# Kernel tuning notes

Hardware: AMD Instinct MI355X
Metric: run time of the kernel (lower is better)

## Reference

```python
import jax, jax.numpy as jnp
import numpy as np

N_NODES = 100000
N_EDGES = 1000000
IN_DIM = 64
HID = 64
OUT = 64
NEG_SLOPE = 0.2  # PyG GATConv default


def setup_inputs() -> dict:
    key = jax.random.key(0)
    ks = jax.random.split(key, 10)
    x = jax.random.normal(ks[0], (N_NODES, IN_DIM), dtype=jnp.float32)
    edge_index = jax.random.randint(ks[1], (2, N_EDGES), 0, N_NODES, dtype=jnp.int64)
    s = 1.0 / np.sqrt(IN_DIM)
    sh = 1.0 / np.sqrt(HID)
    W_src = jax.random.uniform(ks[2], (IN_DIM, HID), jnp.float32, -s, s)
    W_dst = jax.random.uniform(ks[3], (IN_DIM, HID), jnp.float32, -s, s)
    att_src = jax.random.uniform(ks[4], (HID,), jnp.float32, -sh, sh)
    att_dst = jax.random.uniform(ks[5], (HID,), jnp.float32, -sh, sh)
    bias = jnp.zeros((HID,), jnp.float32)
    W_lin = jax.random.uniform(ks[6], (HID, OUT), jnp.float32, -sh, sh)
    b_lin = jax.random.uniform(ks[7], (OUT,), jnp.float32, -sh, sh)
    return {"x": x, "edge_index": edge_index, "W_src": W_src, "W_dst": W_dst,
            "att_src": att_src, "att_dst": att_dst, "bias": bias,
            "W_lin": W_lin, "b_lin": b_lin}


def reference(x, edge_index, W_src, W_dst, att_src, att_dst, bias, W_lin, b_lin):
    src, tgt = edge_index[0], edge_index[1]
    # Bias-free linear projections (PyG GATConv with tuple in_channels)
    h_src = x @ W_src                      # [N, HID]
    h_dst = x @ W_dst                      # [N, HID]
    a_src = h_src @ att_src                # [N]
    a_dst = h_dst @ att_dst                # [N]
    # Per-edge attention logits: LeakyReLU(a_src[j] + a_dst[i])
    e = a_src[src] + a_dst[tgt]            # [E]
    e = jnp.where(e > 0, e, NEG_SLOPE * e)
    # Segment-softmax over incoming edges of each target node
    seg_max = jax.ops.segment_max(e, tgt, num_segments=N_NODES)  # [N]
    expw = jnp.exp(e - seg_max[tgt])                             # [E]
    denom = jax.ops.segment_sum(expw, tgt, num_segments=N_NODES)  # [N]
    alpha = expw / (denom[tgt] + 1e-16)                          # [E]
    # Scatter-aggregate weighted source features
    msgs = alpha[:, None] * h_src[src]                           # [E, HID]
    out = jax.ops.segment_sum(msgs, tgt, num_segments=N_NODES)   # [N, HID]
    out = out + bias
    # Final linear + ReLU
    return jax.nn.relu(out @ W_lin + b_lin)
```

## Files before the change

kernel.cpp:

```cpp
#include <hip/hip_runtime.h>
#include <hip/hip_fp16.h>
#include <math.h>

#define HID 64
#define CBITS 6
#define CSZ 64
#define MAXB 2048
#define CAP 832
#define CAPH 576
#define PB 896
#define MSB 256
#define XSTR 17

__device__ __forceinline__ float4 f4fma(float a, const float4 b, float4 c) {
    c.x = fmaf(a, b.x, c.x); c.y = fmaf(a, b.y, c.y);
    c.z = fmaf(a, b.z, c.z); c.w = fmaf(a, b.w, c.w);
    return c;
}

__global__ void init_kernel(const float* __restrict__ W_dst,
                            const float* __restrict__ att_dst,
                            float* __restrict__ vdst,
                            int* __restrict__ gcursor, int nbc) {
    if (blockIdx.x == 0 && threadIdx.x < HID) {
        int k = threadIdx.x;
        float acc = 0.0f;
#pragma unroll 8
        for (int h = 0; h < HID; ++h) acc = fmaf(W_dst[k * HID + h], att_dst[h], acc);
        vdst[k] = acc;
    }
    int stride = gridDim.x * blockDim.x;
    for (int i = blockIdx.x * blockDim.x + threadIdx.x; i < nbc; i += stride)
        gcursor[i] = i * CAP;
}

__global__ void __launch_bounds__(256)
mid_kernel(const float* __restrict__ x,
           const float* __restrict__ W_src,
           const float* __restrict__ att_src,
           const float* __restrict__ vdst,
           __half* __restrict__ h_half,
           float* __restrict__ a_src,
           float* __restrict__ a_dst, int N,
           const int* __restrict__ src, const int* __restrict__ tgt,
           int* __restrict__ gcursor, int* __restrict__ rec, int E, int nbc) {
    __shared__ __align__(16) char smraw[25600];
    const int t = threadIdx.x;

    if (blockIdx.x < PB) {
        float4* Ws4  = (float4*)smraw;
        float4* att4 = Ws4 + HID * 16;
        float4* vd4  = att4 + 16;
        float4* xs4f = vd4 + 16;

        for (int i = t; i < HID * 16; i += 256) Ws4[i] = ((const float4*)W_src)[i];
        if (t < 16) {
            att4[t] = ((const float4*)att_src)[t];
            vd4[t]  = ((const float4*)vdst)[t];
        }

        const int g0 = t >> 4;
        const int s = t & 15;
        const float4* x4 = (const float4*)x;
        uint2* h2 = (uint2*)h_half;

        for (int base = blockIdx.x * 32; base < N; base += PB * 32) {
            __syncthreads();
#pragma unroll
            for (int u = 0; u < 2; ++u) {
                int f = t + u * 256;
                int node = base + (f >> 4);
                xs4f[(f >> 4) * XSTR + (f & 15)] =
                    (node < N) ? x4[(long long)node * 16 + (f & 15)]
                               : make_float4(0, 0, 0, 0);
            }
            __syncthreads();

            const float4* xr0 = xs4f + g0 * XSTR;
            const float4* xr1 = xs4f + (g0 + 16) * XSTR;

            float4 acc0 = make_float4(0, 0, 0, 0);
            float4 acc1 = make_float4(0, 0, 0, 0);
#pragma unroll 4
            for (int kk = 0; kk < 16; ++kk) {
                float4 xv0 = xr0[kk];
                float4 xv1 = xr1[kk];
                float4 w0 = Ws4[(4 * kk + 0) * 16 + s];
                float4 w1 = Ws4[(4 * kk + 1) * 16 + s];
                float4 w2 = Ws4[(4 * kk + 2) * 16 + s];
                float4 w3 = Ws4[(4 * kk + 3) * 16 + s];
                acc0 = f4fma(xv0.x, w0, acc0);
                acc1 = f4fma(xv1.x, w0, acc1);
                acc0 = f4fma(xv0.y, w1, acc0);
                acc1 = f4fma(xv1.y, w1, acc1);
                acc0 = f4fma(xv0.z, w2, acc0);
                acc1 = f4fma(xv1.z, w2, acc1);
                acc0 = f4fma(xv0.w, w3, acc0);
                acc1 = f4fma(xv1.w, w3, acc1);
            }

            float4 av = att4[s], qv = vd4[s];
            float p0 = acc0.x * av.x + acc0.y * av.y + acc0.z * av.z + acc0.w * av.w;
            float p1 = acc1.x * av.x + acc1.y * av.y + acc1.z * av.z + acc1.w * av.w;
            float4 xq0 = xr0[s];
            float4 xq1 = xr1[s];
            float q0 = xq0.x * qv.x + xq0.y * qv.y + xq0.z * qv.z + xq0.w * qv.w;
            float q1 = xq1.x * qv.x + xq1.y * qv.y + xq1.z * qv.z + xq1.w * qv.w;
#pragma unroll
            for (int off = 1; off < 16; off <<= 1) {
                p0 += __shfl_xor(p0, off, 64);
                p1 += __shfl_xor(p1, off, 64);
                q0 += __shfl_xor(q0, off, 64);
                q1 += __shfl_xor(q1, off, 64);
            }

            int n0 = base + g0, n1 = base + g0 + 16;
            if (n0 < N) {
                __half2 lo = __float22half2_rn(make_float2(acc0.x, acc0.y));
                __half2 hi = __float22half2_rn(make_float2(acc0.z, acc0.w));
                uint2 pk; pk.x = *(unsigned*)&lo; pk.y = *(unsigned*)&hi;
                h2[(long long)n0 * 16 + s] = pk;
                if (s == 0) { a_src[n0] = p0; a_dst[n0] = q0; }
            }
            if (n1 < N) {
                __half2 lo = __float22half2_rn(make_float2(acc1.x, acc1.y));
                __half2 hi = __float22half2_rn(make_float2(acc1.z, acc1.w));
                uint2 pk; pk.x = *(unsigned*)&lo; pk.y = *(unsigned*)&hi;
                h2[(long long)n1 * 16 + s] = pk;
                if (s == 0) { a_src[n1] = p1; a_dst[n1] = q1; }
            }
        }
    } else {
        int* lh = (int*)smraw;
        const int bid = blockIdx.x - PB;

        for (int i = t; i < nbc; i += 256) lh[i] = 0;
        __syncthreads();
        int chunk = (E + MSB - 1) / MSB;
        int e0 = bid * chunk;
        int e1 = min(E, e0 + chunk);
        for (int e = e0 + t; e < e1; e += 256)
            atomicAdd(&lh[tgt[e] >> CBITS], 1);
        __syncthreads();
        for (int i = t; i < nbc; i += 256)
            if (lh[i]) lh[i] = atomicAdd(&gcursor[i], lh[i]);
        __syncthreads();
        for (int e = e0 + t; e < e1; e += 256) {
            int s = src[e], tg = tgt[e];
            int bi = tg >> CBITS;
            int pos = atomicAdd(&lh[bi], 1);
            if (pos < (bi + 1) * CAP)
                rec[pos] = (s << CBITS) | (tg & (CSZ - 1));
        }
    }
}

__global__ void __launch_bounds__(256)
sort_gather_kernel(const int* __restrict__ gcursor, const int* __restrict__ rec,
                   const __half* __restrict__ h_half,
                   const float* __restrict__ a_src, const float* __restrict__ a_dst,
                   const float* __restrict__ bias,
                   const float* __restrict__ W_lin, const float* __restrict__ b_lin,
                   float* __restrict__ out, int N) {
    __shared__ float4 Wl4[HID * 16];
    __shared__ float4 bs4[16], bl4[16];
    __shared__ int ssort[CAPH];
    __shared__ int hist[32];
    __shared__ int loff[33];
    __shared__ int cur[32];
    __shared__ int sd[32];

    const int t = threadIdx.x;
    for (int i = t; i < HID * 16; i += 256) Wl4[i] = ((const float4*)W_lin)[i];
    if (t < 16) {
        bs4[t] = ((const float4*)bias)[t];
        bl4[t] = ((const float4*)b_lin)[t];
    }

    const int bk = blockIdx.x >> 1;
    const int half = blockIdx.x & 1;
    const int node0 = (bk << CBITS) + half * 32;
    const int nn = min(32, N - node0);
    const int beg = bk * CAP;
    int cnt = gcursor[bk] - beg;
    if (cnt > CAP) cnt = CAP;

    if (t < 32) hist[t] = 0;
    __syncthreads();
    for (int j = t; j < cnt; j += 256) {
        int tl = rec[beg + j] & (CSZ - 1);
        if ((tl >> 5) == half) atomicAdd(&hist[tl & 31], 1);
    }
    __syncthreads();
    if (t < 32) sd[t] = hist[t];
    __syncthreads();
    for (int off = 1; off < 32; off <<= 1) {
        int v = (t < 32 && t >= off) ? sd[t - off] : 0;
        __syncthreads();
        if (t < 32) sd[t] += v;
        __syncthreads();
    }
    if (t < 32) {
        int e = sd[t] - hist[t];
        loff[t] = e; cur[t] = e;
        if (t == 31) loff[32] = min(sd[31], CAPH);
    }
    __syncthreads();
    for (int j = t; j < cnt; j += 256) {
        int r = rec[beg + j];
        int tl = r & (CSZ - 1);
        if ((tl >> 5) == half) {
            int pos = atomicAdd(&cur[tl & 31], 1);
            if (pos < CAPH) ssort[pos] = r >> CBITS;
        }
    }
    __syncthreads();

    const int lane = t & 63;
    const int w = t >> 6;
    const int g = lane >> 4;
    const int s = lane & 15;
    const int gbase = g << 4;
    const uint2* h2 = (const uint2*)h_half;
    float4* out4 = (float4*)out;

#pragma unroll 1
    for (int r2 = 0; r2 < 2; ++r2) {
        int nloc = w * 8 + r2 * 4 + g;
        int n = node0 + nloc;
        bool act = (nloc < nn);
        float adn = act ? a_dst[n] : 0.0f;
        int jb = min(loff[nloc], CAPH);
        int je = min(loff[nloc + 1], CAPH);

        float4 acc = make_float4(0, 0, 0, 0);
        float dsum = 0.0f;
        int j = jb;
        for (; j + 4 <= je; j += 4) {
            int s0 = ssort[j], s1 = ssort[j + 1], s2 = ssort[j + 2], s3 = ssort[j + 3];
            uint2 r0 = h2[(long long)s0 * 16 + s];
            uint2 r1 = h2[(long long)s1 * 16 + s];
            uint2 r2v = h2[(long long)s2 * 16 + s];
            uint2 r3 = h2[(long long)s3 * 16 + s];
            float v0 = a_src[s0] + adn, v1 = a_src[s1] + adn;
            float v2 = a_src[s2] + adn, v3 = a_src[s3] + adn;
            v0 = (v0 > 0.0f) ? v0 : 0.2f * v0;
            v1 = (v1 > 0.0f) ? v1 : 0.2f * v1;
            v2 = (v2 > 0.0f) ? v2 : 0.2f * v2;
            v3 = (v3 > 0.0f) ? v3 : 0.2f * v3;
            float w0 = __expf(v0), w1 = __expf(v1);
            float w2 = __expf(v2), w3 = __expf(v3);
            dsum += (w0 + w1) + (w2 + w3);
            float2 f0a = __half22float2(*(const __half2*)&r0.x);
            float2 f0b = __half22float2(*(const __half2*)&r0.y);
            float2 f1a = __half22float2(*(const __half2*)&r1.x);
            float2 f1b = __half22float2(*(const __half2*)&r1.y);
            float2 f2a = __half22float2(*(const __half2*)&r2v.x);
            float2 f2b = __half22float2(*(const __half2*)&r2v.y);
            float2 f3a = __half22float2(*(const __half2*)&r3.x);
            float2 f3b = __half22float2(*(const __half2*)&r3.y);
            acc.x = fmaf(w0, f0a.x, fmaf(w1, f1a.x, fmaf(w2, f2a.x, fmaf(w3, f3a.x, acc.x))));
            acc.y = fmaf(w0, f0a.y, fmaf(w1, f1a.y, fmaf(w2, f2a.y, fmaf(w3, f3a.y, acc.y))));
            acc.z = fmaf(w0, f0b.x, fmaf(w1, f1b.x, fmaf(w2, f2b.x, fmaf(w3, f3b.x, acc.z))));
            acc.w = fmaf(w0, f0b.y, fmaf(w1, f1b.y, fmaf(w2, f2b.y, fmaf(w3, f3b.y, acc.w))));
        }
        for (; j < je; ++j) {
            int s0 = ssort[j];
            uint2 r0 = h2[(long long)s0 * 16 + s];
            float v0 = a_src[s0] + adn;
            v0 = (v0 > 0.0f) ? v0 : 0.2f * v0;
            float w0 = __expf(v0);
            dsum += w0;
            float2 f0a = __half22float2(*(const __half2*)&r0.x);
            float2 f0b = __half22float2(*(const __half2*)&r0.y);
            acc.x = fmaf(w0, f0a.x, acc.x);
            acc.y = fmaf(w0, f0a.y, acc.y);
            acc.z = fmaf(w0, f0b.x, acc.z);
            acc.w = fmaf(w0, f0b.y, acc.w);
        }

        float inv = 1.0f / (dsum + 1e-16f);
        float4 bsv = bs4[s];
        float4 r;
        r.x = fmaf(acc.x, inv, bsv.x);
        r.y = fmaf(acc.y, inv, bsv.y);
        r.z = fmaf(acc.z, inv, bsv.z);
        r.w = fmaf(acc.w, inv, bsv.w);

        float4 o = bl4[s];
#pragma unroll 4
        for (int ks = 0; ks < 16; ++ks) {
            float rx = __shfl(r.x, gbase + ks, 64);
            float ry = __shfl(r.y, gbase + ks, 64);
            float rz = __shfl(r.z, gbase + ks, 64);
            float rw = __shfl(r.w, gbase + ks, 64);
            o = f4fma(rx, Wl4[(4 * ks + 0) * 16 + s], o);
            o = f4fma(ry, Wl4[(4 * ks + 1) * 16 + s], o);
            o = f4fma(rz, Wl4[(4 * ks + 2) * 16 + s], o);
            o = f4fma(rw, Wl4[(4 * ks + 3) * 16 + s], o);
        }

        if (act) {
            float4 res;
            res.x = o.x > 0.0f ? o.x : 0.0f;
            res.y = o.y > 0.0f ? o.y : 0.0f;
            res.z = o.z > 0.0f ? o.z : 0.0f;
            res.w = o.w > 0.0f ? o.w : 0.0f;
            out4[(long long)n * 16 + s] = res;
        }
    }
}

extern "C" void kernel_launch(void* const* d_in, const int* in_sizes, int n_in,
                              void* d_out, int out_size, void* d_ws, size_t ws_size,
                              hipStream_t stream) {
    const float* x       = (const float*)d_in[0];
    const int*   edge    = (const int*)d_in[1];
    const float* W_src   = (const float*)d_in[2];
    const float* W_dst   = (const float*)d_in[3];
    const float* att_src = (const float*)d_in[4];
    const float* att_dst = (const float*)d_in[5];
    const float* bias    = (const float*)d_in[6];
    const float* W_lin   = (const float*)d_in[7];
    const float* b_lin   = (const float*)d_in[8];
    float* out = (float*)d_out;

    const int N = in_sizes[0] / HID;
    const int E = in_sizes[1] / 2;
    const int* src = edge;
    const int* tgt = edge + E;
    const int nbc = (N + CSZ - 1) / CSZ;

    __half* h_half  = (__half*)d_ws;
    float*  a_src   = (float*)(h_half + (size_t)N * HID);
    float*  a_dst   = a_src + N;
    float*  vdst    = a_dst + N;
    int*    gcursor = (int*)(vdst + 64);
    int*    rec     = gcursor + MAXB;

    init_kernel<<<8, 256, 0, stream>>>(W_dst, att_dst, vdst, gcursor, nbc);
    mid_kernel<<<PB + MSB, 256, 0, stream>>>(x, W_src, att_src, vdst, h_half,
                                             a_src, a_dst, N,
                                             src, tgt, gcursor, rec, E, nbc);
    sort_gather_kernel<<<nbc * 2, 256, 0, stream>>>(gcursor, rec, h_half, a_src, a_dst,
                                                    bias, W_lin, b_lin, out, N);
}
```

Before: 163.0 us.

## Drop init kernel, fold vdst into mid kernel, one gather block per bucket

Removes the separate init kernel. Each projection block now computes the W_dst·att_dst vector itself, and the bucket cursors are zeroed with a memset and hold relative offsets. The sort-gather kernel now uses one block per 64-node bucket instead of two half-buckets, so each bucket's records are read and scanned once. The 32-entry shared-memory prefix scan becomes a wavefront shuffle scan. In exchange the grid has half as many blocks, each doing more serial work, and the redundant per-block vdst compute adds a little work to every projection block.

```diff
diff --git a/kernel.cpp b/kernel.cpp
--- a/kernel.cpp
+++ b/kernel.cpp
@@ -7,7 +7,6 @@
 #define CSZ 64
 #define MAXB 2048
 #define CAP 832
-#define CAPH 576
 #define PB 896
 #define MSB 256
 #define XSTR 17
@@ -18,27 +17,12 @@
     return c;
 }
 
-__global__ void init_kernel(const float* __restrict__ W_dst,
-                            const float* __restrict__ att_dst,
-                            float* __restrict__ vdst,
-                            int* __restrict__ gcursor, int nbc) {
-    if (blockIdx.x == 0 && threadIdx.x < HID) {
-        int k = threadIdx.x;
-        float acc = 0.0f;
-#pragma unroll 8
-        for (int h = 0; h < HID; ++h) acc = fmaf(W_dst[k * HID + h], att_dst[h], acc);
-        vdst[k] = acc;
-    }
-    int stride = gridDim.x * blockDim.x;
-    for (int i = blockIdx.x * blockDim.x + threadIdx.x; i < nbc; i += stride)
-        gcursor[i] = i * CAP;
-}
-
 __global__ void __launch_bounds__(256)
 mid_kernel(const float* __restrict__ x,
            const float* __restrict__ W_src,
+           const float* __restrict__ W_dst,
            const float* __restrict__ att_src,
-           const float* __restrict__ vdst,
+           const float* __restrict__ att_dst,
            __half* __restrict__ h_half,
            float* __restrict__ a_src,
            float* __restrict__ a_dst, int N,
@@ -54,9 +38,13 @@
         float4* xs4f = vd4 + 16;
 
         for (int i = t; i < HID * 16; i += 256) Ws4[i] = ((const float4*)W_src)[i];
-        if (t < 16) {
-            att4[t] = ((const float4*)att_src)[t];
-            vd4[t]  = ((const float4*)vdst)[t];
+        if (t < 16) att4[t] = ((const float4*)att_src)[t];
+        if (t < HID) {
+            float acc = 0.0f;
+#pragma unroll 8
+            for (int h = 0; h < HID; ++h)
+                acc = fmaf(W_dst[t * HID + h], att_dst[h], acc);
+            ((float*)vd4)[t] = acc;
         }
 
         const int g0 = t >> 4;
@@ -143,7 +131,7 @@
             atomicAdd(&lh[tgt[e] >> CBITS], 1);
         __syncthreads();
         for (int i = t; i < nbc; i += 256)
-            if (lh[i]) lh[i] = atomicAdd(&gcursor[i], lh[i]);
+            if (lh[i]) lh[i] = i * CAP + atomicAdd(&gcursor[i], lh[i]);
         __syncthreads();
         for (int e = e0 + t; e < e1; e += 256) {
             int s = src[e], tg = tgt[e];
@@ -164,11 +152,10 @@
                    float* __restrict__ out, int N) {
     __shared__ float4 Wl4[HID * 16];
     __shared__ float4 bs4[16], bl4[16];
-    __shared__ int ssort[CAPH];
-    __shared__ int hist[32];
-    __shared__ int loff[33];
-    __shared__ int cur[32];
-    __shared__ int sd[32];
+    __shared__ int ssort[CAP];
+    __shared__ int hist[CSZ];
+    __shared__ int loff[CSZ + 1];
+    __shared__ int cur[CSZ];
 
     const int t = threadIdx.x;
     for (int i = t; i < HID * 16; i += 256) Wl4[i] = ((const float4*)W_lin)[i];
@@ -177,42 +164,35 @@
         bl4[t] = ((const float4*)b_lin)[t];
     }
 
-    const int bk = blockIdx.x >> 1;
-    const int half = blockIdx.x & 1;
-    const int node0 = (bk << CBITS) + half * 32;
-    const int nn = min(32, N - node0);
+    const int bk = blockIdx.x;
+    const int node0 = bk << CBITS;
+    const int nn = min(CSZ, N - node0);
     const int beg = bk * CAP;
-    int cnt = gcursor[bk] - beg;
+    int cnt = gcursor[bk];
     if (cnt > CAP) cnt = CAP;
 
-    if (t < 32) hist[t] = 0;
+    if (t < CSZ) hist[t] = 0;
     __syncthreads();
-    for (int j = t; j < cnt; j += 256) {
-        int tl = rec[beg + j] & (CSZ - 1);
-        if ((tl >> 5) == half) atomicAdd(&hist[tl & 31], 1);
-    }
+    for (int j = t; j < cnt; j += 256)
+        atomicAdd(&hist[rec[beg + j] & (CSZ - 1)], 1);
     __syncthreads();
-    if (t < 32) sd[t] = hist[t];
-    __syncthreads();
-    for (int off = 1; off < 32; off <<= 1) {
-        int v = (t < 32 && t >= off) ? sd[t - off] : 0;
-        __syncthreads();
-        if (t < 32) sd[t] += v;
-        __syncthreads();
-    }
-    if (t < 32) {
-        int e = sd[t] - hist[t];
-        loff[t] = e; cur[t] = e;
-        if (t == 31) loff[32] = min(sd[31], CAPH);
+    if (t < CSZ) {
+        int h = hist[t];
+        int v = h;
+#pragma unroll
+        for (int off = 1; off < CSZ; off <<= 1) {
+            int u = __shfl_up(v, off, 64);
+            if (t >= off) v += u;
+        }
+        loff[t] = v - h;
+        cur[t]  = v - h;
+        if (t == CSZ - 1) loff[CSZ] = v;
     }
     __syncthreads();
     for (int j = t; j < cnt; j += 256) {
         int r = rec[beg + j];
-        int tl = r & (CSZ - 1);
-        if ((tl >> 5) == half) {
-            int pos = atomicAdd(&cur[tl & 31], 1);
-            if (pos < CAPH) ssort[pos] = r >> CBITS;
-        }
+        int pos = atomicAdd(&cur[r & (CSZ - 1)], 1);
+        ssort[pos] = r >> CBITS;
     }
     __syncthreads();
 
@@ -225,13 +205,13 @@
     float4* out4 = (float4*)out;
 
 #pragma unroll 1
-    for (int r2 = 0; r2 < 2; ++r2) {
-        int nloc = w * 8 + r2 * 4 + g;
+    for (int r2 = 0; r2 < 4; ++r2) {
+        int nloc = w * 16 + r2 * 4 + g;
         int n = node0 + nloc;
         bool act = (nloc < nn);
         float adn = act ? a_dst[n] : 0.0f;
-        int jb = min(loff[nloc], CAPH);
-        int je = min(loff[nloc + 1], CAPH);
+        int jb = loff[nloc];
+        int je = loff[nloc + 1];
 
         float4 acc = make_float4(0, 0, 0, 0);
         float dsum = 0.0f;
@@ -334,14 +314,13 @@
     __half* h_half  = (__half*)d_ws;
     float*  a_src   = (float*)(h_half + (size_t)N * HID);
     float*  a_dst   = a_src + N;
-    float*  vdst    = a_dst + N;
-    int*    gcursor = (int*)(vdst + 64);
+    int*    gcursor = (int*)(a_dst + N);
     int*    rec     = gcursor + MAXB;
 
-    init_kernel<<<8, 256, 0, stream>>>(W_dst, att_dst, vdst, gcursor, nbc);
-    mid_kernel<<<PB + MSB, 256, 0, stream>>>(x, W_src, att_src, vdst, h_half,
-                                             a_src, a_dst, N,
+    hipMemsetAsync(gcursor, 0, MAXB * sizeof(int), stream);
+    mid_kernel<<<PB + MSB, 256, 0, stream>>>(x, W_src, W_dst, att_src, att_dst,
+                                             h_half, a_src, a_dst, N,
                                              src, tgt, gcursor, rec, E, nbc);
-    sort_gather_kernel<<<nbc * 2, 256, 0, stream>>>(gcursor, rec, h_half, a_src, a_dst,
-                                                    bias, W_lin, b_lin, out, N);
+    sort_gather_kernel<<<nbc, 256, 0, stream>>>(gcursor, rec, h_half, a_src, a_dst,
+                                                bias, W_lin, b_lin, out, N);
 }
```

Result: slower. 166.9 us (+2.4%).
